# Optimization experiments

Hardware: AMD Instinct MI355X
Metric: run time of the kernel (lower is better)

The kernel has to match this reference:

```python
import jax, jax.numpy as jnp
import numpy as np
import math

B, N, CS, CZ = 1, 512, 384, 128
GD = 16            # ipa_conf.c_hidden -> num 3D groups G
CH = GD * 3        # per-head hidden = 48
H = 8
PQ, PV = 8, 12
NF = 4             # num_frequencies
INF, EPS = 1e5, 1e-8
CZ4 = CZ // 4


def base_frequencies(num_freqs=NF, base=8.0, max_freq=1.0):
    fs = [min(base ** (-2 * i / num_freqs) * max_freq, max_freq) for i in range(num_freqs)]
    return jnp.asarray(fs, dtype=jnp.float32)


def hat(v):
    # v: [..., 3] -> skew-symmetric [..., 3, 3]
    x, y, z = v[..., 0], v[..., 1], v[..., 2]
    o = jnp.zeros_like(x)
    return jnp.stack([
        jnp.stack([o, -z, y], -1),
        jnp.stack([z, o, -x], -1),
        jnp.stack([-y, x, o], -1)], -2)


def setup_inputs() -> dict:
    key = jax.random.key(0)
    ks = jax.random.split(key, 24)
    std = 0.02
    hc = CH * H
    hpkv = H * (PQ + PV) * 3
    inp = {
        's': jax.random.normal(ks[0], (B, N, CS), jnp.float32),
        'z': jax.random.normal(ks[1], (B, N, N, CZ), jnp.float32),
        'rotvec': jax.random.normal(ks[2], (B, N, 3), jnp.float32),
        'mask': jnp.ones((B, N), jnp.float32),
        'wq': jax.random.normal(ks[3], (CS, hc), jnp.float32) * std,
        'bq': jnp.zeros((hc,), jnp.float32),
        'wkv': jax.random.normal(ks[4], (CS, 2 * hc), jnp.float32) * std,
        'bkv': jnp.zeros((2 * hc,), jnp.float32),
        'wkvp': jax.random.normal(ks[5], (CS, hpkv), jnp.float32) * std,
        'bkvp': jnp.zeros((hpkv,), jnp.float32),
        'wb': jax.random.normal(ks[6], (CZ, H), jnp.float32) * std,
        'bb': jnp.zeros((H,), jnp.float32),
        'wdz': jax.random.normal(ks[7], (CZ, CZ4), jnp.float32) * std,
        'bdz': jnp.zeros((CZ4,), jnp.float32),
        'wout': jax.random.normal(ks[8], (H * (CZ4 + CH + PV * 4), CS), jnp.float32) * std,
        'bout': jnp.zeros((CS,), jnp.float32),
        'log_freq_adj': jax.random.normal(ks[9], (NF,), jnp.float32) * std,
        'group_weights': jax.random.normal(ks[10], (GD,), jnp.float32) * std,
        'freq_weights': jnp.full((NF,), 1.0 / NF, jnp.float32),
    }
    return inp


def reference(s, z, rotvec, mask, wq, bq, wkv, bkv, wkvp, bkvp, wb, bb,
              wdz, bdz, wout, bout, log_freq_adj, group_weights, freq_weights):
    G = GD
    # projections
    q = (s @ wq + bq).reshape(B, N, H, CH)
    kv = (s @ wkv + bkv).reshape(B, N, H, 2 * CH)
    k, v = kv[..., :CH], kv[..., CH:]
    P = PQ + PV
    kvp = (s @ wkvp + bkvp).reshape(B, N, 3, H * P)      # torch split(...,3)+stack(-1)
    kvp = jnp.moveaxis(kvp, -2, -1).reshape(B, N, H, P, 3)
    v_pts = kvp[..., PQ:, :]                             # [B,N,H,PV,3]
    bias = z @ wb + bb                                   # [B,N,N,H]
    # RoPE-inspired multi-frequency Rodrigues rotations
    nrm = jnp.linalg.norm(rotvec, axis=-1, keepdims=True)
    angle = nrm + 1e-8                                   # [B,N,1]
    axis = rotvec / jnp.maximum(nrm, 1e-12)
    freqs = base_frequencies() * jnp.exp(log_freq_adj)   # [F]
    theta = angle * freqs                                # [B,N,F]
    K = hat(axis)                                        # [B,N,3,3]
    K2 = K @ K
    sin_t = jnp.sin(theta)[..., None, None]              # [B,N,F,1,1]
    cos_t = jnp.cos(theta)[..., None, None]
    I3 = jnp.eye(3, dtype=s.dtype)
    R = I3 + sin_t * K[:, :, None] + (1.0 - cos_t) * K2[:, :, None]  # [B,N,F,3,3]
    qg = q.reshape(B, N, H, G, 3)
    kg = k.reshape(B, N, H, G, 3)
    q_rot = jnp.einsum('bnfij,bnhgj->bnhgfi', R, qg)     # [B,N,H,G,F,3]
    k_rot = jnp.einsum('bnfij,bnhgj->bnhgfi', R, kg)
    # aggregation weights (sum over groups, softmax-weighted freqs)
    freq_w = jax.nn.softmax(freq_weights)
    group_w = jax.nn.softplus(group_weights) * math.sqrt(1.0 / G)
    qw = q_rot * freq_w[None, None, None, None, :, None] * group_w[None, None, None, :, None, None]
    scores = jnp.einsum('bihgfc,bjhgfc->bhij', qw, k_rot) / math.sqrt(3.0)
    a = scores + math.sqrt(1.0 / 3.0) * jnp.transpose(bias, (0, 3, 1, 2))
    sq_mask = INF * (mask[:, :, None] * mask[:, None, :] - 1.0)
    a = jax.nn.softmax(a + sq_mask[:, None], axis=-1)    # [B,H,N,N]
    # outputs
    o = jnp.einsum('bhij,bjhc->bihc', a, v).reshape(B, N, H * CH)
    o_pt = jnp.einsum('bhij,bjhpc->bihpc', a, v_pts)     # [B,N,H,PV,3]
    o_pt_norm = jnp.sqrt(jnp.sum(o_pt ** 2, -1) + EPS).reshape(B, N, H * PV)
    o_pt_flat = o_pt.reshape(B, N, H * PV, 3)
    pair_z = z @ wdz + bdz                               # [B,N,N,CZ4]
    o_pair = jnp.einsum('bhij,bijc->bihc', a, pair_z).reshape(B, N, H * CZ4)
    feats = jnp.concatenate([o, o_pt_flat[..., 0], o_pt_flat[..., 1],
                             o_pt_flat[..., 2], o_pt_norm, o_pair], axis=-1)
    return feats @ wout + bout                           # [B,N,CS]
```

## Files before the change

### kernel.cpp

```cpp
#include <hip/hip_runtime.h>
#include <hip/hip_bf16.h>
#include <math.h>


#define OFF_PROJ 0
#define SZ_PROJ (512*1632)
#define OFF_QW (OFF_PROJ + SZ_PROJ)
#define SZ_QW (8*512*192)
#define OFF_KST (OFF_QW + SZ_QW)
#define OFF_VCAT (OFF_KST + SZ_QW)
#define SZ_VCAT (512*768)
#define OFF_A (OFF_VCAT + SZ_VCAT)
#define SZ_A (8*512*512)
#define OFF_PZ (OFF_A + SZ_A)
#define SZ_PZ (512*512*32/2)
#define OFF_FEATS (OFF_PZ + SZ_PZ)
#define SZ_FEATS (512*1024)
#define OFF_PART (OFF_FEATS + SZ_FEATS)
#define SZ_PART (8*512*384)

__global__ __launch_bounds__(256) void proj_kernel(
    const float* __restrict__ s, const float* __restrict__ wq, const float* __restrict__ bq,
    const float* __restrict__ wkv, const float* __restrict__ bkv,
    const float* __restrict__ wkvp, const float* __restrict__ bkvp,
    float* __restrict__ proj)
{
  __shared__ float sT[384][34];
  int ct = blockIdx.x;
  int i0 = blockIdx.y * 32;
  int col0 = ct * 64;
  const float* W; const float* bias; int wld, wcol0;
  if (col0 < 384)       { W = wq;   bias = bq;   wld = 384; wcol0 = col0; }
  else if (col0 < 1152) { W = wkv;  bias = bkv;  wld = 768; wcol0 = col0 - 384; }
  else                  { W = wkvp; bias = bkvp; wld = 480; wcol0 = col0 - 1152; }
  int t = threadIdx.x;
  #pragma unroll
  for (int r = 0; r < 12; r++){
    int e = t + 256*r;
    int i = e & 31;
    int k4 = e >> 5;
    float4 v = *(const float4*)(s + (size_t)(i0 + i)*384 + k4*4);
    sT[k4*4+0][i] = v.x; sT[k4*4+1][i] = v.y; sT[k4*4+2][i] = v.z; sT[k4*4+3][i] = v.w;
  }
  __syncthreads();
  int cr = t & 15;
  int ipair = t >> 4;
  int ii = ipair * 2;
  int wc = wcol0 + cr*4;
  bool valid = (wc + 4 <= wld);
  int wcc = valid ? wc : (wld - 4);
  float acc[2][4];
  #pragma unroll
  for (int q = 0; q < 2; q++)
    #pragma unroll
    for (int p = 0; p < 4; p++) acc[q][p] = 0.f;
  #pragma unroll 4
  for (int k = 0; k < 384; k++){
    float2 a2 = *(const float2*)&sT[k][ii];
    float4 w4 = *(const float4*)(W + (size_t)k*wld + wcc);
    acc[0][0] = fmaf(a2.x, w4.x, acc[0][0]);
    acc[0][1] = fmaf(a2.x, w4.y, acc[0][1]);
    acc[0][2] = fmaf(a2.x, w4.z, acc[0][2]);
    acc[0][3] = fmaf(a2.x, w4.w, acc[0][3]);
    acc[1][0] = fmaf(a2.y, w4.x, acc[1][0]);
    acc[1][1] = fmaf(a2.y, w4.y, acc[1][1]);
    acc[1][2] = fmaf(a2.y, w4.z, acc[1][2]);
    acc[1][3] = fmaf(a2.y, w4.w, acc[1][3]);
  }
  if (valid){
    float4 bv = *(const float4*)(bias + wc);
    #pragma unroll
    for (int q = 0; q < 2; q++){
      int row = i0 + ii + q;
      float4 o;
      o.x = acc[q][0] + bv.x; o.y = acc[q][1] + bv.y;
      o.z = acc[q][2] + bv.z; o.w = acc[q][3] + bv.w;
      *(float4*)(proj + (size_t)row*1632 + col0 + cr*4) = o;
    }
  }
}

__global__ __launch_bounds__(128) void node_kernel(
    const float* __restrict__ proj, const float* __restrict__ rotvec,
    const float* __restrict__ lfa, const float* __restrict__ gwts, const float* __restrict__ fwts,
    float* __restrict__ Qw, float* __restrict__ Kst, float* __restrict__ Vcat)
{
  int i = blockIdx.x, t = threadIdx.x;
  const float* pr = proj + (size_t)i*1632;
  float rx = rotvec[i*3], ry = rotvec[i*3+1], rz = rotvec[i*3+2];
  float nrm = sqrtf(rx*rx + ry*ry + rz*rz);
  float angle = nrm + 1e-8f;
  float inv = 1.0f / fmaxf(nrm, 1e-12f);
  float ax = rx*inv, ay = ry*inv, az = rz*inv;
  float f0 = fwts[0], f1 = fwts[1], f2 = fwts[2], f3 = fwts[3];
  float mfw = fmaxf(fmaxf(f0,f1), fmaxf(f2,f3));
  float e0 = expf(f0-mfw), e1 = expf(f1-mfw), e2 = expf(f2-mfw), e3 = expf(f3-mfw);
  float esum = e0+e1+e2+e3;
  float fw[4] = {e0/esum, e1/esum, e2/esum, e3/esum};
  float fq[4] = { 1.0f*expf(lfa[0]), 0.35355339059327373f*expf(lfa[1]),
                  0.125f*expf(lfa[2]), 0.04419417382415922f*expf(lfa[3]) };
  int h = t >> 4, g = t & 15;
  float gw = log1pf(expf(gwts[g])) * 0.25f;
  float q0 = pr[h*48 + g*3 + 0], q1 = pr[h*48 + g*3 + 1], q2 = pr[h*48 + g*3 + 2];
  float k0 = pr[384 + h*96 + g*3 + 0], k1 = pr[384 + h*96 + g*3 + 1], k2 = pr[384 + h*96 + g*3 + 2];
  #pragma unroll
  for (int f = 0; f < 4; f++){
    float th = angle * fq[f];
    float sn = sinf(th), cs = cosf(th), omc = 1.0f - cs;
    float r00 = cs + omc*ax*ax,       r01 = omc*ax*ay - sn*az,  r02 = omc*ax*az + sn*ay;
    float r10 = omc*ay*ax + sn*az,    r11 = cs + omc*ay*ay,     r12 = omc*ay*az - sn*ax;
    float r20 = omc*az*ax - sn*ay,    r21 = omc*az*ay + sn*ax,  r22 = cs + omc*az*az;
    float qr0 = r00*q0 + r01*q1 + r02*q2;
    float qr1 = r10*q0 + r11*q1 + r12*q2;
    float qr2 = r20*q0 + r21*q1 + r22*q2;
    float kr0 = r00*k0 + r01*k1 + r02*k2;
    float kr1 = r10*k0 + r11*k1 + r12*k2;
    float kr2 = r20*k0 + r21*k1 + r22*k2;
    float sc = fw[f] * gw * 0.57735026918962576f;
    int base = (h*512 + i)*192 + (g*4 + f)*3;
    Qw[base+0] = qr0*sc; Qw[base+1] = qr1*sc; Qw[base+2] = qr2*sc;
    Kst[base+0] = kr0;   Kst[base+1] = kr1;   Kst[base+2] = kr2;
  }
  for (int c = t; c < 384; c += 128){
    int hh = c / 48, cc = c % 48;
    Vcat[(size_t)i*768 + hh*96 + cc] = pr[384 + hh*96 + 48 + cc];
  }
  for (int e = t; e < 288; e += 128){
    int hh = e / 36, r = e % 36;
    int p = r / 3, axv = r % 3;
    Vcat[(size_t)i*768 + hh*96 + 48 + p*3 + axv] = pr[1152 + axv*160 + hh*20 + 8 + p];
  }
}

#define ZPLANE 584
__global__ __launch_bounds__(256) void zbias_pz_kernel(
    const float* __restrict__ z, const float* __restrict__ wb, const float* __restrict__ bb,
    const float* __restrict__ wdz, const float* __restrict__ bdz,
    float* __restrict__ biasS, ushort* __restrict__ PZ)
{
  __shared__ float zs[8*ZPLANE];
  __shared__ float Wl[40*132];
  int i = blockIdx.y;
  int jt = blockIdx.x;
  int t = threadIdx.x;
  for (int e = t; e < 40*128; e += 256){
    int ch = e % 40, k = e / 40;
    Wl[ch*132 + k] = (ch < 8) ? wb[k*8 + ch] : wdz[k*32 + (ch - 8)];
  }
  int cg = t >> 6, jg = t & 63;
  int ch0 = cg*10;
  float acc[10][2];
  #pragma unroll
  for (int cc = 0; cc < 10; cc++){ acc[cc][0] = 0.f; acc[cc][1] = 0.f; }
  const float* zrow = z + ((size_t)i*512 + jt*128)*128;
  int a0 = jg*4 + (jg>>3)*4;
  int j1 = 64 + jg;
  int a1 = j1*4 + (j1>>3)*4;
  for (int kt = 0; kt < 4; kt++){
    __syncthreads();
    #pragma unroll
    for (int r = 0; r < 4; r++){
      int idx = t + 256*r;
      int kq = idx & 7, j = idx >> 3;
      float4 v = *(const float4*)(zrow + (size_t)j*128 + kt*32 + kq*4);
      *(float4*)&zs[kq*ZPLANE + j*4 + (j>>3)*4] = v;
    }
    __syncthreads();
    #pragma unroll
    for (int kq = 0; kq < 8; kq++){
      float4 z0 = *(const float4*)&zs[kq*ZPLANE + a0];
      float4 z1 = *(const float4*)&zs[kq*ZPLANE + a1];
      #pragma unroll
      for (int cc = 0; cc < 10; cc++){
        float4 w = *(const float4*)&Wl[(ch0+cc)*132 + kt*32 + kq*4];
        acc[cc][0] = fmaf(z0.x, w.x, acc[cc][0]);
        acc[cc][0] = fmaf(z0.y, w.y, acc[cc][0]);
        acc[cc][0] = fmaf(z0.z, w.z, acc[cc][0]);
        acc[cc][0] = fmaf(z0.w, w.w, acc[cc][0]);
        acc[cc][1] = fmaf(z1.x, w.x, acc[cc][1]);
        acc[cc][1] = fmaf(z1.y, w.y, acc[cc][1]);
        acc[cc][1] = fmaf(z1.z, w.z, acc[cc][1]);
        acc[cc][1] = fmaf(z1.w, w.w, acc[cc][1]);
      }
    }
  }
  #pragma unroll
  for (int cc = 0; cc < 10; cc++){
    int ch = ch0 + cc;
    if (ch < 8){
      float b = bb[ch];
      float* bp = biasS + (size_t)ch*262144 + i*512 + jt*128 + jg;
      bp[0]  = 0.57735026918962576f * (acc[cc][0] + b);
      bp[64] = 0.57735026918962576f * (acc[cc][1] + b);
    } else {
      int c = ch - 8;
      float b = bdz[c];
      ushort* pp = PZ + ((size_t)i*32 + c)*512 + jt*128 + jg;
      __hip_bfloat16 v0 = __float2bfloat16(acc[cc][0] + b);
      __hip_bfloat16 v1 = __float2bfloat16(acc[cc][1] + b);
      pp[0]  = *(ushort*)&v0;
      pp[64] = *(ushort*)&v1;
    }
  }
}

#define KPLANE 2312
__global__ __launch_bounds__(256) void scores_kernel(
    const float* __restrict__ Qw, const float* __restrict__ Kst,
    const float* __restrict__ mask, float* A)
{
  __shared__ float Ks[4*KPLANE];
  __shared__ float Qs[4*40];
  int i0 = blockIdx.x * 8;
  int h = blockIdx.y;
  int t = threadIdx.x;
  int ig = t >> 6, jl = t & 63;
  const float* Kb = Kst + (size_t)h*512*192;
  const float* Qb = Qw + (size_t)(h*512 + i0)*192;
  float acc[2][8];
  float mj[8];
  #pragma unroll
  for (int jt = 0; jt < 8; jt++) mj[jt] = mask[jt*64 + jl];
  #pragma unroll
  for (int q = 0; q < 2; q++){
    int i = i0 + ig*2 + q;
    float mi = mask[i];
    #pragma unroll
    for (int jt = 0; jt < 8; jt++){
      acc[q][jt] = A[((size_t)h*512 + i)*512 + jt*64 + jl] + 100000.0f*(mi*mj[jt] - 1.0f);
    }
  }
  int ja[8];
  #pragma unroll
  for (int jt = 0; jt < 8; jt++){
    int j = jt*64 + jl;
    ja[jt] = j*4 + (j>>3)*4;
  }
  for (int kc = 0; kc < 12; kc++){
    __syncthreads();
    {
      int k4 = t >> 6;
      #pragma unroll
      for (int r = 0; r < 8; r++){
        int j = (t & 63) + 64*r;
        float4 v = *(const float4*)(Kb + (size_t)j*192 + kc*16 + k4*4);
        *(float4*)&Ks[k4*KPLANE + j*4 + (j>>3)*4] = v;
      }
    }
    if (t < 32){
      int qi = t >> 2, k4 = t & 3;
      float4 v = *(const float4*)(Qb + (size_t)qi*192 + kc*16 + k4*4);
      *(float4*)&Qs[k4*40 + qi*4] = v;
    }
    __syncthreads();
    #pragma unroll
    for (int k4 = 0; k4 < 4; k4++){
      float4 qf[2];
      #pragma unroll
      for (int q = 0; q < 2; q++)
        qf[q] = *(const float4*)&Qs[k4*40 + (ig*2+q)*4];
      #pragma unroll
      for (int jt = 0; jt < 8; jt++){
        float4 kf = *(const float4*)&Ks[k4*KPLANE + ja[jt]];
        #pragma unroll
        for (int q = 0; q < 2; q++){
          acc[q][jt] = fmaf(qf[q].x, kf.x, acc[q][jt]);
          acc[q][jt] = fmaf(qf[q].y, kf.y, acc[q][jt]);
          acc[q][jt] = fmaf(qf[q].z, kf.z, acc[q][jt]);
          acc[q][jt] = fmaf(qf[q].w, kf.w, acc[q][jt]);
        }
      }
    }
  }
  #pragma unroll
  for (int q = 0; q < 2; q++){
    int i = i0 + ig*2 + q;
    float m = acc[q][0];
    #pragma unroll
    for (int jt = 1; jt < 8; jt++) m = fmaxf(m, acc[q][jt]);
    for (int off = 32; off > 0; off >>= 1) m = fmaxf(m, __shfl_xor(m, off));
    float ssum = 0.f;
    #pragma unroll
    for (int jt = 0; jt < 8; jt++){ acc[q][jt] = expf(acc[q][jt] - m); ssum += acc[q][jt]; }
    for (int off = 32; off > 0; off >>= 1) ssum += __shfl_xor(ssum, off);
    float invs = 1.0f / ssum;
    #pragma unroll
    for (int jt = 0; jt < 8; jt++){
      A[((size_t)h*512 + i)*512 + jt*64 + jl] = acc[q][jt] * invs;
    }
  }
}

__global__ __launch_bounds__(256) void opair_kernel(
    const float* __restrict__ A, const ushort* __restrict__ PZ,
    float* __restrict__ feats)
{
  __shared__ float a_s[512*10];
  int i = blockIdx.x;
  int t = threadIdx.x;
  #pragma unroll
  for (int r = 0; r < 4; r++){
    int idx = t + r*256;
    int h = idx >> 7, j4 = idx & 127;
    float4 v = *(const float4*)(A + ((size_t)h*512 + i)*512 + j4*4);
    a_s[(j4*4+0)*10 + h] = v.x;
    a_s[(j4*4+1)*10 + h] = v.y;
    a_s[(j4*4+2)*10 + h] = v.z;
    a_s[(j4*4+3)*10 + h] = v.w;
  }
  __syncthreads();
  int h = t >> 5, c = t & 31;
  const ushort* pzb = PZ + ((size_t)i*32 + c)*512;
  const float* ap = a_s + h;
  float acc = 0.f;
  #pragma unroll 8
  for (int j4 = 0; j4 < 128; j4++){
    ushort4 p4 = *(const ushort4*)(pzb + j4*4);
    float z0 = __uint_as_float((unsigned)p4.x << 16);
    float z1 = __uint_as_float((unsigned)p4.y << 16);
    float z2 = __uint_as_float((unsigned)p4.z << 16);
    float z3 = __uint_as_float((unsigned)p4.w << 16);
    acc = fmaf(ap[(j4*4+0)*10], z0, acc);
    acc = fmaf(ap[(j4*4+1)*10], z1, acc);
    acc = fmaf(ap[(j4*4+2)*10], z2, acc);
    acc = fmaf(ap[(j4*4+3)*10], z3, acc);
  }
  feats[(size_t)i*1024 + 768 + h*32 + c] = acc;
}

__global__ __launch_bounds__(256) void ovgemm_kernel(
    const float* __restrict__ A, const float* __restrict__ Vcat,
    float* __restrict__ feats)
{
  __shared__ float A_s[64*18];
  __shared__ float V_s[64*100];
  __shared__ float opt[16*40];
  int i0 = blockIdx.x * 16;
  int h = blockIdx.y;
  int t = threadIdx.x;
  int ip = t >> 5;
  int cg = t & 31;
  float acc[2][4];
  #pragma unroll
  for (int q = 0; q < 2; q++)
    #pragma unroll
    for (int m = 0; m < 4; m++) acc[q][m] = 0.f;
  for (int cb = 0; cb < 512; cb += 64){
    __syncthreads();
    {
      int ii = t >> 4, j4 = t & 15;
      float4 v = *(const float4*)(A + ((size_t)h*512 + i0 + ii)*512 + cb + j4*4);
      A_s[(j4*4+0)*18 + ii] = v.x;
      A_s[(j4*4+1)*18 + ii] = v.y;
      A_s[(j4*4+2)*18 + ii] = v.z;
      A_s[(j4*4+3)*18 + ii] = v.w;
    }
    #pragma unroll
    for (int r = 0; r < 6; r++){
      int idx = t + r*256;
      int j = idx / 24, cq = idx % 24;
      float4 v = *(const float4*)(Vcat + (size_t)(cb + j)*768 + h*96 + cq*4);
      *(float4*)&V_s[j*100 + cq*4] = v;
    }
    __syncthreads();
    #pragma unroll 4
    for (int k = 0; k < 64; k++){
      float2 a2 = *(const float2*)&A_s[k*18 + ip*2];
      float4 v4 = *(const float4*)&V_s[k*100 + cg*4];
      acc[0][0] = fmaf(a2.x, v4.x, acc[0][0]);
      acc[0][1] = fmaf(a2.x, v4.y, acc[0][1]);
      acc[0][2] = fmaf(a2.x, v4.z, acc[0][2]);
      acc[0][3] = fmaf(a2.x, v4.w, acc[0][3]);
      acc[1][0] = fmaf(a2.y, v4.x, acc[1][0]);
      acc[1][1] = fmaf(a2.y, v4.y, acc[1][1]);
      acc[1][2] = fmaf(a2.y, v4.z, acc[1][2]);
      acc[1][3] = fmaf(a2.y, v4.w, acc[1][3]);
    }
  }
  int c0 = cg*4;
  if (c0 < 48){
    #pragma unroll
    for (int q = 0; q < 2; q++){
      *(float4*)&feats[(size_t)(i0 + ip*2 + q)*1024 + h*48 + c0] =
        make_float4(acc[q][0], acc[q][1], acc[q][2], acc[q][3]);
    }
  } else if (c0 < 84){
    #pragma unroll
    for (int q = 0; q < 2; q++){
      #pragma unroll
      for (int m = 0; m < 4; m++){
        opt[(ip*2+q)*40 + (c0 - 48 + m)] = acc[q][m];
      }
    }
  }
  __syncthreads();
  if (t < 192){
    int il = t / 12, p = t % 12;
    float x = opt[il*40 + p*3], y = opt[il*40 + p*3 + 1], zz = opt[il*40 + p*3 + 2];
    float* fr = feats + (size_t)(i0 + il)*1024;
    fr[384 + h*12 + p] = x;
    fr[480 + h*12 + p] = y;
    fr[576 + h*12 + p] = zz;
    fr[672 + h*12 + p] = sqrtf(x*x + y*y + zz*zz + 1e-8f);
  }
}

__global__ __launch_bounds__(256) void outgemm_kernel(
    const float* __restrict__ feats, const float* __restrict__ wout,
    float* __restrict__ part)
{
  __shared__ float fA[32*68];
  __shared__ float fB[32*68];
  int ct = blockIdx.x;
  int it = blockIdx.y;
  int sk = blockIdx.z;
  int i0 = it*64, c0 = ct*64, k0 = sk*128;
  int t = threadIdx.x;
  int ir = t >> 4, cr = t & 15;
  float acc[4][4];
  #pragma unroll
  for (int q = 0; q < 4; q++)
    #pragma unroll
    for (int p = 0; p < 4; p++) acc[q][p] = 0.f;
  for (int kt = 0; kt < 128; kt += 32){
    __syncthreads();
    #pragma unroll
    for (int r = 0; r < 2; r++){
      int e = t + 256*r;
      int i = e & 63, kq = e >> 6;
      float4 v = *(const float4*)(feats + (size_t)(i0 + i)*1024 + k0 + kt + kq*4);
      fA[(kq*4+0)*68 + i] = v.x; fA[(kq*4+1)*68 + i] = v.y;
      fA[(kq*4+2)*68 + i] = v.z; fA[(kq*4+3)*68 + i] = v.w;
    }
    #pragma unroll
    for (int r = 0; r < 2; r++){
      int e = t + 256*r;
      int kk = e >> 4, c4 = e & 15;
      float4 v = *(const float4*)(wout + (size_t)(k0 + kt + kk)*384 + c0 + c4*4);
      *(float4*)&fB[kk*68 + c4*4] = v;
    }
    __syncthreads();
    #pragma unroll 8
    for (int k = 0; k < 32; k++){
      float4 a4 = *(const float4*)&fA[k*68 + ir*4];
      float4 b4 = *(const float4*)&fB[k*68 + cr*4];
      acc[0][0] = fmaf(a4.x, b4.x, acc[0][0]);
      acc[0][1] = fmaf(a4.x, b4.y, acc[0][1]);
      acc[0][2] = fmaf(a4.x, b4.z, acc[0][2]);
      acc[0][3] = fmaf(a4.x, b4.w, acc[0][3]);
      acc[1][0] = fmaf(a4.y, b4.x, acc[1][0]);
      acc[1][1] = fmaf(a4.y, b4.y, acc[1][1]);
      acc[1][2] = fmaf(a4.y, b4.z, acc[1][2]);
      acc[1][3] = fmaf(a4.y, b4.w, acc[1][3]);
      acc[2][0] = fmaf(a4.z, b4.x, acc[2][0]);
      acc[2][1] = fmaf(a4.z, b4.y, acc[2][1]);
      acc[2][2] = fmaf(a4.z, b4.z, acc[2][2]);
      acc[2][3] = fmaf(a4.z, b4.w, acc[2][3]);
      acc[3][0] = fmaf(a4.w, b4.x, acc[3][0]);
      acc[3][1] = fmaf(a4.w, b4.y, acc[3][1]);
      acc[3][2] = fmaf(a4.w, b4.z, acc[3][2]);
      acc[3][3] = fmaf(a4.w, b4.w, acc[3][3]);
    }
  }
  float* pb = part + ((size_t)sk*512 + i0)*384 + c0;
  #pragma unroll
  for (int q = 0; q < 4; q++){
    float4 o;
    o.x = acc[q][0]; o.y = acc[q][1]; o.z = acc[q][2]; o.w = acc[q][3];
    *(float4*)&pb[(size_t)(ir*4 + q)*384 + cr*4] = o;
  }
}

__global__ __launch_bounds__(256) void outreduce_kernel(
    const float* __restrict__ part, const float* __restrict__ bout,
    float* __restrict__ out)
{
  int e = blockIdx.x*256 + threadIdx.x;
  float4 acc = *(const float4*)(bout + (e % 96)*4);
  #pragma unroll
  for (int sk = 0; sk < 8; sk++){
    float4 p = *(const float4*)(part + (size_t)sk*196608 + (size_t)e*4);
    acc.x += p.x; acc.y += p.y; acc.z += p.z; acc.w += p.w;
  }
  *(float4*)(out + (size_t)e*4) = acc;
}

extern "C" void kernel_launch(void* const* d_in, const int* in_sizes, int n_in,
                              void* d_out, int out_size, void* d_ws, size_t ws_size,
                              hipStream_t stream)
{
  const float* s    = (const float*)d_in[0];
  const float* z    = (const float*)d_in[1];
  const float* rotv = (const float*)d_in[2];
  const float* mask = (const float*)d_in[3];
  const float* wq   = (const float*)d_in[4];
  const float* bq   = (const float*)d_in[5];
  const float* wkv  = (const float*)d_in[6];
  const float* bkv  = (const float*)d_in[7];
  const float* wkvp = (const float*)d_in[8];
  const float* bkvp = (const float*)d_in[9];
  const float* wb   = (const float*)d_in[10];
  const float* bb   = (const float*)d_in[11];
  const float* wdz  = (const float*)d_in[12];
  const float* bdz  = (const float*)d_in[13];
  const float* wout = (const float*)d_in[14];
  const float* bout = (const float*)d_in[15];
  const float* lfa  = (const float*)d_in[16];
  const float* gwts = (const float*)d_in[17];
  const float* fwts = (const float*)d_in[18];
  float* out = (float*)d_out;
  float* ws  = (float*)d_ws;

  float* proj  = ws + OFF_PROJ;
  float* Qw    = ws + OFF_QW;
  float* Kst   = ws + OFF_KST;
  float* Vcat  = ws + OFF_VCAT;
  float* A     = ws + OFF_A;
  ushort* PZ   = (ushort*)(ws + OFF_PZ);
  float* feats = ws + OFF_FEATS;
  float* part  = ws + OFF_PART;

  proj_kernel     <<<dim3(26, 16), 256, 0, stream>>>(s, wq, bq, wkv, bkv, wkvp, bkvp, proj);
  node_kernel     <<<dim3(512),    128, 0, stream>>>(proj, rotv, lfa, gwts, fwts, Qw, Kst, Vcat);
  zbias_pz_kernel <<<dim3(4, 512), 256, 0, stream>>>(z, wb, bb, wdz, bdz, A, PZ);
  scores_kernel   <<<dim3(64, 8),  256, 0, stream>>>(Qw, Kst, mask, A);
  opair_kernel    <<<dim3(512),    256, 0, stream>>>(A, PZ, feats);
  ovgemm_kernel   <<<dim3(32, 8),  256, 0, stream>>>(A, Vcat, feats);
  outgemm_kernel  <<<dim3(6, 8, 8),256, 0, stream>>>(feats, wout, part);
  outreduce_kernel<<<dim3(192),    256, 0, stream>>>(part, bout, out);
}
```

Measured before the change: 391.0 us.

## Remap z projection kernel to one pair column per thread with all 40 channels

```diff
diff --git a/kernel.cpp b/kernel.cpp
--- a/kernel.cpp
+++ b/kernel.cpp
@@ -132,13 +132,12 @@
   }
 }
 
-#define ZPLANE 584
 __global__ __launch_bounds__(256) void zbias_pz_kernel(
     const float* __restrict__ z, const float* __restrict__ wb, const float* __restrict__ bb,
     const float* __restrict__ wdz, const float* __restrict__ bdz,
     float* __restrict__ biasS, ushort* __restrict__ PZ)
 {
-  __shared__ float zs[8*ZPLANE];
+  __shared__ float zs[256*20];
   __shared__ float Wl[40*132];
   int i = blockIdx.y;
   int jt = blockIdx.x;
@@ -147,60 +146,43 @@
     int ch = e % 40, k = e / 40;
     Wl[ch*132 + k] = (ch < 8) ? wb[k*8 + ch] : wdz[k*32 + (ch - 8)];
   }
-  int cg = t >> 6, jg = t & 63;
-  int ch0 = cg*10;
-  float acc[10][2];
-  #pragma unroll
-  for (int cc = 0; cc < 10; cc++){ acc[cc][0] = 0.f; acc[cc][1] = 0.f; }
-  const float* zrow = z + ((size_t)i*512 + jt*128)*128;
-  int a0 = jg*4 + (jg>>3)*4;
-  int j1 = 64 + jg;
-  int a1 = j1*4 + (j1>>3)*4;
-  for (int kt = 0; kt < 4; kt++){
+  float acc[40];
+  #pragma unroll
+  for (int ch = 0; ch < 40; ch++) acc[ch] = 0.f;
+  const float* zrow = z + ((size_t)i*512 + jt*256)*128;
+  for (int kt = 0; kt < 8; kt++){
     __syncthreads();
     #pragma unroll
     for (int r = 0; r < 4; r++){
       int idx = t + 256*r;
-      int kq = idx & 7, j = idx >> 3;
-      float4 v = *(const float4*)(zrow + (size_t)j*128 + kt*32 + kq*4);
-      *(float4*)&zs[kq*ZPLANE + j*4 + (j>>3)*4] = v;
-    }
-    __syncthreads();
-    #pragma unroll
-    for (int kq = 0; kq < 8; kq++){
-      float4 z0 = *(const float4*)&zs[kq*ZPLANE + a0];
-      float4 z1 = *(const float4*)&zs[kq*ZPLANE + a1];
+      int kq = idx & 3, j = idx >> 2;
+      float4 v = *(const float4*)(zrow + (size_t)j*128 + kt*16 + kq*4);
+      *(float4*)&zs[j*20 + kq*4] = v;
+    }
+    __syncthreads();
+    #pragma unroll
+    for (int kq = 0; kq < 4; kq++){
+      float4 z4 = *(const float4*)&zs[t*20 + kq*4];
+      const float* wl = Wl + kt*16 + kq*4;
       #pragma unroll
-      for (int cc = 0; cc < 10; cc++){
-        float4 w = *(const float4*)&Wl[(ch0+cc)*132 + kt*32 + kq*4];
-        acc[cc][0] = fmaf(z0.x, w.x, acc[cc][0]);
-        acc[cc][0] = fmaf(z0.y, w.y, acc[cc][0]);
-        acc[cc][0] = fmaf(z0.z, w.z, acc[cc][0]);
-        acc[cc][0] = fmaf(z0.w, w.w, acc[cc][0]);
-        acc[cc][1] = fmaf(z1.x, w.x, acc[cc][1]);
-        acc[cc][1] = fmaf(z1.y, w.y, acc[cc][1]);
-        acc[cc][1] = fmaf(z1.z, w.z, acc[cc][1]);
-        acc[cc][1] = fmaf(z1.w, w.w, acc[cc][1]);
+      for (int ch = 0; ch < 40; ch++){
+        float4 w4 = *(const float4*)(wl + ch*132);
+        acc[ch] = fmaf(z4.x, w4.x, acc[ch]);
+        acc[ch] = fmaf(z4.y, w4.y, acc[ch]);
+        acc[ch] = fmaf(z4.z, w4.z, acc[ch]);
+        acc[ch] = fmaf(z4.w, w4.w, acc[ch]);
       }
     }
   }
-  #pragma unroll
-  for (int cc = 0; cc < 10; cc++){
-    int ch = ch0 + cc;
-    if (ch < 8){
-      float b = bb[ch];
-      float* bp = biasS + (size_t)ch*262144 + i*512 + jt*128 + jg;
-      bp[0]  = 0.57735026918962576f * (acc[cc][0] + b);
-      bp[64] = 0.57735026918962576f * (acc[cc][1] + b);
-    } else {
-      int c = ch - 8;
-      float b = bdz[c];
-      ushort* pp = PZ + ((size_t)i*32 + c)*512 + jt*128 + jg;
-      __hip_bfloat16 v0 = __float2bfloat16(acc[cc][0] + b);
-      __hip_bfloat16 v1 = __float2bfloat16(acc[cc][1] + b);
-      pp[0]  = *(ushort*)&v0;
-      pp[64] = *(ushort*)&v1;
-    }
+  int j = jt*256 + t;
+  #pragma unroll
+  for (int ch = 0; ch < 8; ch++){
+    biasS[(size_t)ch*262144 + i*512 + j] = 0.57735026918962576f * (acc[ch] + bb[ch]);
+  }
+  #pragma unroll
+  for (int c = 0; c < 32; c++){
+    __hip_bfloat16 v = __float2bfloat16(acc[8 + c] + bdz[c]);
+    PZ[((size_t)i*32 + c)*512 + j] = *(ushort*)&v;
   }
 }
 
@@ -522,7 +504,7 @@
 
   proj_kernel     <<<dim3(26, 16), 256, 0, stream>>>(s, wq, bq, wkv, bkv, wkvp, bkvp, proj);
   node_kernel     <<<dim3(512),    128, 0, stream>>>(proj, rotv, lfa, gwts, fwts, Qw, Kst, Vcat);
-  zbias_pz_kernel <<<dim3(4, 512), 256, 0, stream>>>(z, wb, bb, wdz, bdz, A, PZ);
+  zbias_pz_kernel <<<dim3(2, 512), 256, 0, stream>>>(z, wb, bb, wdz, bdz, A, PZ);
   scores_kernel   <<<dim3(64, 8),  256, 0, stream>>>(Qw, Kst, mask, A);
   opair_kernel    <<<dim3(512),    256, 0, stream>>>(A, PZ, feats);
   ovgemm_kernel   <<<dim3(32, 8),  256, 0, stream>>>(A, Vcat, feats);
```

Result: slower. 452.8 us (+15.8%).
